# Performance work log

Hardware: AMD Instinct MI355X
Metric: run time of the kernel (lower is better)

Reference implementation:

```python
import jax, jax.numpy as jnp
import numpy as np

EPS = 1e-5
NEG_INF = -9e15  # matches torch's -9000000000000000.0 mask fill


def layer_norm(x, g, b):
    mu = jnp.mean(x, axis=-1, keepdims=True)
    var = jnp.mean((x - mu) ** 2, axis=-1, keepdims=True)
    return (x - mu) / jnp.sqrt(var + EPS) * g + b


def setup_inputs() -> dict:
    key = jax.random.key(0)
    n, C, Cout, K = 8192, 128, 128, 2
    ks = jax.random.split(key, 5)
    x = jax.random.normal(ks[0], (n, C), dtype=jnp.float32)
    adj = jax.random.randint(ks[1], (n, n), 0, 2).astype(jnp.float32)  # 0/1 adjacency
    s = 1.0 / np.sqrt(C)
    # W0[i]: applied as h = x @ W0[i]  (== torch Linear(C,C,bias=False))
    W0 = jax.random.uniform(ks[2], (K, C, C), dtype=jnp.float32, minval=-s, maxval=s)
    W1 = jax.random.uniform(ks[3], (K, C, Cout), dtype=jnp.float32, minval=-s, maxval=s)
    sa = 1.0 / np.sqrt(2 * C)
    a = jax.random.uniform(ks[4], (K, 2 * C), dtype=jnp.float32, minval=-sa, maxval=sa)
    ln1_g = jnp.ones((C,), jnp.float32); ln1_b = jnp.zeros((C,), jnp.float32)
    ln2_g = jnp.ones((C,), jnp.float32); ln2_b = jnp.zeros((C,), jnp.float32)
    return {"x": x, "adj": adj, "W0": W0, "W1": W1, "a": a,
            "ln1_g": ln1_g, "ln1_b": ln1_b, "ln2_g": ln2_g, "ln2_b": ln2_b}


def reference(x, adj, W0, W1, a, ln1_g, ln1_b, ln2_g, ln2_b):
    n, C = x.shape
    K = W0.shape[0]
    Cout = W1.shape[-1]
    # adj + eye (repeated) only feeds `> 0`; equivalent fixed mask:
    mask = (adj > 0) | jnp.eye(n, dtype=bool)
    x_norm = layer_norm(x, ln1_g, ln1_b)
    h_next = jnp.zeros((n, Cout), dtype=x.dtype)
    atten_agg = jnp.zeros((n, n), dtype=x.dtype)
    for i in range(K):
        h = x_norm @ W0[i]                                   # (n, C)
        a_l, a_r = a[i, :C], a[i, C:]
        # h_cross[i,j] = [h[i], h[j]]; linear decomposes exactly:
        e = jax.nn.leaky_relu(h @ a_l[:, None] + (h @ a_r)[None, :])  # (n, n)
        e = jnp.where(mask, e, NEG_INF)
        atten = jax.nn.softmax(e, axis=1)                    # row-stochastic
        attn_h = atten @ h                                   # (n, C)
        attn_h = attn_h + x                                  # residual=True
        attn_h = layer_norm(attn_h, ln2_g, ln2_b)
        h_next = h_next + jax.nn.elu(attn_h @ W1[i]) / K
        atten_agg = atten_agg + atten / K
    return h_next, atten_agg
```

## Files before the change

kernel.cpp:

```cpp
#include <hip/hip_runtime.h>
#include <stdint.h>

#define N 8192
#define C 128

typedef float f32x4 __attribute__((ext_vector_type(4)));
typedef short bf16x8 __attribute__((ext_vector_type(8)));

__device__ __forceinline__ float wred(float v){
#pragma unroll
  for(int o=32;o;o>>=1) v += __shfl_xor(v,o);
  return v;
}
__device__ __forceinline__ unsigned short f2bf(float x){
  union{float f; unsigned u;} c; c.f = x;
  unsigned u = c.u;
  u += 0x7fffu + ((u>>16)&1u);
  return (unsigned short)(u>>16);
}
__device__ __forceinline__ float lrelu(float z){ return z>0.f ? z : 0.01f*z; }

__global__ void k_front(const float* __restrict__ x, const float* __restrict__ g1,
                        const float* __restrict__ b1, const float* __restrict__ W0,
                        const float* __restrict__ a, unsigned short* __restrict__ hB,
                        float* __restrict__ hl, float* __restrict__ hr){
  __shared__ __align__(16) float xn[32*132];
  __shared__ __align__(16) float ws[C*C];
  __shared__ __align__(16) float hs[32*C];
  int t = threadIdx.x, l = t & 63, w = t >> 6;
  int r0 = blockIdx.x*32;
#pragma unroll
  for(int p=0;p<8;p++){
    int row = p*4 + w;
    const float2 xv = *(const float2*)(x + (size_t)(r0+row)*C + l*2);
    float mu = wred(xv.x + xv.y) * (1.f/C);
    float dx = xv.x - mu, dy = xv.y - mu;
    float var = wred(dx*dx + dy*dy) * (1.f/C);
    float rs = rsqrtf(var + 1e-5f);
    const float2 gv = *(const float2*)(g1 + l*2);
    const float2 bv = *(const float2*)(b1 + l*2);
    xn[row*132 + l*2]     = dx*rs*gv.x + bv.x;
    xn[row*132 + l*2 + 1] = dy*rs*gv.y + bv.y;
  }
  int cq = t & 31, rq = t >> 5;
  for(int k=0;k<2;k++){
    __syncthreads();
    const float4* wsrc = (const float4*)(W0 + (size_t)k*C*C);
    float4* wdst = (float4*)ws;
#pragma unroll
    for(int r=0;r<16;r++) wdst[t + r*256] = wsrc[t + r*256];
    __syncthreads();
    float4 acc[4] = {};
    const float4* ws4 = (const float4*)ws;
#pragma unroll 4
    for(int kk=0; kk<C; ++kk){
      float4 wv = ws4[kk*32 + cq];
#pragma unroll
      for(int r=0;r<4;r++){
        float xv = xn[(rq*4+r)*132 + kk];
        acc[r].x += xv*wv.x; acc[r].y += xv*wv.y; acc[r].z += xv*wv.z; acc[r].w += xv*wv.w;
      }
    }
    const float4 al = *(const float4*)(a + k*2*C + cq*4);
    const float4 ar = *(const float4*)(a + k*2*C + C + cq*4);
#pragma unroll
    for(int r=0;r<4;r++){
      float sl = acc[r].x*al.x + acc[r].y*al.y + acc[r].z*al.z + acc[r].w*al.w;
      float sr = acc[r].x*ar.x + acc[r].y*ar.y + acc[r].z*ar.z + acc[r].w*ar.w;
#pragma unroll
      for(int o=16;o;o>>=1){ sl += __shfl_xor(sl,o); sr += __shfl_xor(sr,o); }
      if(cq==0){
        hl[k*N + r0 + rq*4 + r] = sl;
        hr[k*N + r0 + rq*4 + r] = sr;
      }
    }
#pragma unroll
    for(int r=0;r<4;r++) *(float4*)(hs + (rq*4+r)*C + cq*4) = acc[r];
    __syncthreads();
    unsigned short tv[16];
#pragma unroll
    for(int q=0;q<16;q++){
      int f = t*16 + q;
      int cb = f>>9, l2 = (f>>3)&63, tt = f&7;
      tv[q] = f2bf(hs[((l2>>4)*8 + tt)*C + cb*16 + (l2&15)]);
    }
    uint4* dst = (uint4*)(hB + (size_t)(k*256 + blockIdx.x)*4096 + t*16);
    dst[0] = *(uint4*)&tv[0];
    dst[1] = *(uint4*)&tv[8];
  }
}

__global__ void k_denom(const float* __restrict__ adj, const float* __restrict__ hl,
                        const float* __restrict__ hr, float* __restrict__ invd,
                        unsigned char* __restrict__ maskG){
  int t = threadIdx.x, l = t & 63, w = t >> 6;
  int i = blockIdx.x*8 + w;
  float hl0 = hl[i], hl1 = hl[N+i];
  const float4* arow = (const float4*)(adj + (size_t)i*N);
  float s0 = 0.f, s1 = 0.f;
  for(int it=0; it<16; ++it){
    int j0 = it*512 + l*8;
    float4 a0 = arow[j0/4], a1 = arow[j0/4 + 1];
    float4 h00 = *(const float4*)(hr + j0);
    float4 h01 = *(const float4*)(hr + j0 + 4);
    float4 h10 = *(const float4*)(hr + N + j0);
    float4 h11 = *(const float4*)(hr + N + j0 + 4);
    float av[8]  = {a0.x,a0.y,a0.z,a0.w, a1.x,a1.y,a1.z,a1.w};
    float h0v[8] = {h00.x,h00.y,h00.z,h00.w, h01.x,h01.y,h01.z,h01.w};
    float h1v[8] = {h10.x,h10.y,h10.z,h10.w, h11.x,h11.y,h11.z,h11.w};
    unsigned mb = 0;
#pragma unroll
    for(int tt=0; tt<8; ++tt){
      bool m = (av[tt] > 0.f) || (j0+tt == i);
      mb |= ((unsigned)m) << tt;
      float e0 = __expf(lrelu(hl0 + h0v[tt]));
      float e1 = __expf(lrelu(hl1 + h1v[tt]));
      s0 += m ? e0 : 0.f;
      s1 += m ? e1 : 0.f;
    }
    maskG[(size_t)i*1024 + it*64 + l] = (unsigned char)mb;
  }
  s0 = wred(s0); s1 = wred(s1);
  if(l==0){ invd[i] = 1.f/s0; invd[N+i] = 1.f/s1; }
}

__global__ __launch_bounds__(256, 3)
void k_main(const unsigned char* __restrict__ maskG, const float* __restrict__ hl,
            const float* __restrict__ hr, const float* __restrict__ invd,
            const unsigned short* __restrict__ hB,
            float* __restrict__ agg, float* __restrict__ pvp){
  __shared__ __align__(16) uint4 hBs[2][1024];
  __shared__ __align__(16) float hrs[4096];
  int t = threadIdx.x, l = t & 63, w = t >> 6;
  int r0 = blockIdx.x*64, ch = blockIdx.y;
  int g = l >> 4;
  int lr = w*16 + (l & 15);
  int i = r0 + lr;
  {
    int f0 = t*16, k0 = f0 >> 11, j0 = f0 & 2047;
    const float* src = hr + k0*N + ch*2048 + j0;
#pragma unroll
    for(int q=0;q<4;q++) *(float4*)(hrs + f0 + q*4) = *(const float4*)(src + q*4);
  }
  float hl0 = hl[i], hl1 = hl[N+i];
  float id0 = invd[i], id1 = invd[N+i];
  float* grow = agg + (size_t)i*N + ch*2048;
  const unsigned char* mrow = maskG + (size_t)i*1024 + ch*256;
  const uint4* hBu = (const uint4*)hB;
  f32x4 acc[2][8] = {};
  {
    size_t jn = (size_t)(ch*64)*512;
    hBs[0][t]       = hBu[jn + t];
    hBs[0][t + 256] = hBu[jn + t + 256];
    hBs[0][t + 512] = hBu[131072 + jn + t];
    hBs[0][t + 768] = hBu[131072 + jn + t + 256];
  }
  uint4 rB0, rB1, rB2, rB3;
  {
    size_t jn = (size_t)(ch*64 + 1)*512;
    rB0 = hBu[jn + t];           rB1 = hBu[jn + t + 256];
    rB2 = hBu[131072 + jn + t];  rB3 = hBu[131072 + jn + t + 256];
  }
  unsigned mb  = mrow[g];
  unsigned mbn = mrow[4 + g];
  __syncthreads();
  for(int js=0; js<64; ++js){
    int cur = js & 1;
    int jl = js*32 + g*8;
    float4 h00 = *(const float4*)(hrs + jl);
    float4 h01 = *(const float4*)(hrs + jl + 4);
    float4 h10 = *(const float4*)(hrs + 2048 + jl);
    float4 h11 = *(const float4*)(hrs + 2048 + jl + 4);
    float h0v[8] = {h00.x,h00.y,h00.z,h00.w, h01.x,h01.y,h01.z,h01.w};
    float h1v[8] = {h10.x,h10.y,h10.z,h10.w, h11.x,h11.y,h11.z,h11.w};
    float p0[8], p1[8];
#pragma unroll
    for(int tt=0; tt<8; ++tt){
      bool m = (mb >> tt) & 1;
      float e0 = __expf(lrelu(hl0 + h0v[tt]));
      float e1 = __expf(lrelu(hl1 + h1v[tt]));
      p0[tt] = m ? e0 : 0.f;
      p1[tt] = m ? e1 : 0.f;
    }
    float4 g0, g1;
    g0.x = (p0[0]*id0 + p1[0]*id1)*0.5f;
    g0.y = (p0[1]*id0 + p1[1]*id1)*0.5f;
    g0.z = (p0[2]*id0 + p1[2]*id1)*0.5f;
    g0.w = (p0[3]*id0 + p1[3]*id1)*0.5f;
    g1.x = (p0[4]*id0 + p1[4]*id1)*0.5f;
    g1.y = (p0[5]*id0 + p1[5]*id1)*0.5f;
    g1.z = (p0[6]*id0 + p1[6]*id1)*0.5f;
    g1.w = (p0[7]*id0 + p1[7]*id1)*0.5f;
    *(float4*)(grow + jl)     = g0;
    *(float4*)(grow + jl + 4) = g1;
    union { bf16x8 v; unsigned u[4]; } fu0, fu1;
#pragma unroll
    for(int q=0;q<4;q++){
      asm("v_cvt_pk_bf16_f32 %0, %1, %2" : "=v"(fu0.u[q]) : "v"(p0[2*q]), "v"(p0[2*q+1]));
      asm("v_cvt_pk_bf16_f32 %0, %1, %2" : "=v"(fu1.u[q]) : "v"(p1[2*q]), "v"(p1[2*q+1]));
    }
    const unsigned short* bptr = (const unsigned short*)&hBs[cur][0];
#pragma unroll
    for(int cb=0; cb<8; ++cb){
      bf16x8 b0 = *(const bf16x8*)(bptr + (cb*64 + l)*8);
      bf16x8 b1 = *(const bf16x8*)(bptr + 4096 + (cb*64 + l)*8);
      acc[0][cb] = __builtin_amdgcn_mfma_f32_16x16x32_bf16(fu0.v, b0, acc[0][cb], 0, 0, 0);
      acc[1][cb] = __builtin_amdgcn_mfma_f32_16x16x32_bf16(fu1.v, b1, acc[1][cb], 0, 0, 0);
    }
    if(js < 63){
      uint4* dstb = &hBs[cur ^ 1][0];
      dstb[t]       = rB0;
      dstb[t + 256] = rB1;
      dstb[t + 512] = rB2;
      dstb[t + 768] = rB3;
    }
    unsigned mbn2 = 0;
    if(js < 62){
      size_t jn = (size_t)(ch*64 + js + 2)*512;
      rB0 = hBu[jn + t];           rB1 = hBu[jn + t + 256];
      rB2 = hBu[131072 + jn + t];  rB3 = hBu[131072 + jn + t + 256];
      mbn2 = mrow[(js+2)*4 + g];
    }
    mb = mbn; mbn = mbn2;
    __syncthreads();
  }
#pragma unroll
  for(int k=0;k<2;k++)
#pragma unroll
    for(int cb=0;cb<8;cb++)
#pragma unroll
      for(int r=0;r<4;r++){
        int ig = r0 + w*16 + ((l>>4)<<2) + r;
        int c = cb*16 + (l & 15);
        pvp[(size_t)((ch*2 + k)*N + ig)*C + c] = acc[k][cb][r];
      }
}

__global__ void k_reduce_ln(const float* __restrict__ pvp, const float* __restrict__ invd,
                            const float* __restrict__ x, const float* __restrict__ g2,
                            const float* __restrict__ b2, float* __restrict__ tmp){
  int l = threadIdx.x & 63, w = threadIdx.x >> 6;
  int wid = blockIdx.x*4 + w;
  int k = wid >> 13, i = wid & (N-1);
  float s0 = 0.f, s1 = 0.f;
#pragma unroll
  for(int ch=0; ch<4; ++ch){
    const float2 v = *(const float2*)(pvp + (size_t)((ch*2+k)*N + i)*C + l*2);
    s0 += v.x; s1 += v.y;
  }
  float idv = invd[k*N + i];
  const float2 xv = *(const float2*)(x + (size_t)i*C + l*2);
  float a0 = s0*idv + xv.x, a1 = s1*idv + xv.y;
  float mu = wred(a0 + a1) * (1.f/C);
  float d0 = a0 - mu, d1 = a1 - mu;
  float var = wred(d0*d0 + d1*d1) * (1.f/C);
  float rs = rsqrtf(var + 1e-5f);
  const float2 gv = *(const float2*)(g2 + l*2);
  const float2 bv = *(const float2*)(b2 + l*2);
  float2 o; o.x = d0*rs*gv.x + bv.x; o.y = d1*rs*gv.y + bv.y;
  *(float2*)(tmp + (size_t)k*N*C + (size_t)i*C + l*2) = o;
}

__global__ void k_out(const float* __restrict__ tmp, const float* __restrict__ W1,
                      float* __restrict__ out){
  __shared__ __align__(16) float ws[C*C];
  __shared__ __align__(16) float xs[32*132];
  int t = threadIdx.x, r0 = blockIdx.x*32;
  int cq = t & 31, rq = t >> 5;
  float oacc[4][4] = {};
  for(int k=0;k<2;k++){
    __syncthreads();
    const float4* wsrc = (const float4*)(W1 + (size_t)k*C*C);
    float4* wdst = (float4*)ws;
#pragma unroll
    for(int r=0;r<16;r++) wdst[t + r*256] = wsrc[t + r*256];
    const float4* xsrc = (const float4*)(tmp + (size_t)k*N*C + (size_t)r0*C);
#pragma unroll
    for(int r=0;r<4;r++){
      int f = t + r*256;
      int row = f >> 5, c4 = f & 31;
      *(float4*)(xs + row*132 + c4*4) = xsrc[f];
    }
    __syncthreads();
    float4 acc[4] = {};
    const float4* ws4 = (const float4*)ws;
#pragma unroll 4
    for(int kk=0; kk<C; ++kk){
      float4 wv = ws4[kk*32 + cq];
#pragma unroll
      for(int r=0;r<4;r++){
        float xv = xs[(rq*4+r)*132 + kk];
        acc[r].x += xv*wv.x; acc[r].y += xv*wv.y; acc[r].z += xv*wv.z; acc[r].w += xv*wv.w;
      }
    }
#pragma unroll
    for(int r=0;r<4;r++){
      float* ac = (float*)&acc[r];
#pragma unroll
      for(int cc=0;cc<4;cc++){
        float v = ac[cc];
        v = v > 0.f ? v : (__expf(v) - 1.f);
        oacc[r][cc] += 0.5f*v;
      }
    }
  }
#pragma unroll
  for(int r=0;r<4;r++){
    float4 o = make_float4(oacc[r][0], oacc[r][1], oacc[r][2], oacc[r][3]);
    *(float4*)(out + (size_t)(r0+rq*4+r)*C + cq*4) = o;
  }
}

extern "C" void kernel_launch(void* const* d_in, const int* in_sizes, int n_in,
                              void* d_out, int out_size, void* d_ws, size_t ws_size,
                              hipStream_t stream){
  const float* x   = (const float*)d_in[0];
  const float* adj = (const float*)d_in[1];
  const float* W0  = (const float*)d_in[2];
  const float* W1  = (const float*)d_in[3];
  const float* a   = (const float*)d_in[4];
  const float* g1  = (const float*)d_in[5];
  const float* b1  = (const float*)d_in[6];
  const float* g2  = (const float*)d_in[7];
  const float* b2  = (const float*)d_in[8];
  float* out = (float*)d_out;
  float* ws  = (float*)d_ws;

  unsigned short* hB = (unsigned short*)ws;
  float* hl   = ws + 1048576;
  float* hr   = ws + 1064960;
  float* invd = ws + 1081344;
  float* tmp  = ws + 1097728;
  float* pvp  = ws + 3194880;
  unsigned char* maskG = (unsigned char*)(ws + 19972096);
  float* agg  = out + (size_t)N*C;

  k_front    <<<N/32, 256, 0, stream>>>(x, g1, b1, W0, a, hB, hl, hr);
  k_denom    <<<N/8, 512, 0, stream>>>(adj, hl, hr, invd, maskG);
  k_main     <<<dim3(128, 4), 256, 0, stream>>>(maskG, hl, hr, invd, hB, agg, pvp);
  k_reduce_ln<<<(2*N)/4, 256, 0, stream>>>(pvp, invd, x, g2, b2, tmp);
  k_out      <<<N/32, 256, 0, stream>>>(tmp, W1, out);
}
```

Measured before the change: 272.0 us.

## Split k_main column range into eight chunks and lighten the loop barrier

Doubles the column split of the attention-times-h kernel from 4 to 8 chunks, giving 1024 blocks instead of 512 and half the per-block LDS for hr. Occupancy hint rises to 4 blocks per CU. The reduce kernel now sums 8 partials. The loop-end __syncthreads becomes an explicit lgkmcnt wait plus a raw s_barrier, and the last prefetch wraps around instead of being guarded. The cost is twice the partial-output traffic through pvp and one redundant global prefetch at the end of each block.

```diff
diff --git a/kernel.cpp b/kernel.cpp
--- a/kernel.cpp
+++ b/kernel.cpp
@@ -124,53 +124,55 @@
   if(l==0){ invd[i] = 1.f/s0; invd[N+i] = 1.f/s1; }
 }
 
-__global__ __launch_bounds__(256, 3)
+__global__ __launch_bounds__(256, 4)
 void k_main(const unsigned char* __restrict__ maskG, const float* __restrict__ hl,
             const float* __restrict__ hr, const float* __restrict__ invd,
             const unsigned short* __restrict__ hB,
             float* __restrict__ agg, float* __restrict__ pvp){
   __shared__ __align__(16) uint4 hBs[2][1024];
-  __shared__ __align__(16) float hrs[4096];
+  __shared__ __align__(16) float hrs[2048];
   int t = threadIdx.x, l = t & 63, w = t >> 6;
   int r0 = blockIdx.x*64, ch = blockIdx.y;
   int g = l >> 4;
   int lr = w*16 + (l & 15);
   int i = r0 + lr;
   {
-    int f0 = t*16, k0 = f0 >> 11, j0 = f0 & 2047;
-    const float* src = hr + k0*N + ch*2048 + j0;
-#pragma unroll
-    for(int q=0;q<4;q++) *(float4*)(hrs + f0 + q*4) = *(const float4*)(src + q*4);
+    int f0 = t*8, k0 = f0 >> 10, j0 = f0 & 1023;
+    const float* src = hr + k0*N + ch*1024 + j0;
+    *(float4*)(hrs + f0)     = *(const float4*)src;
+    *(float4*)(hrs + f0 + 4) = *(const float4*)(src + 4);
   }
   float hl0 = hl[i], hl1 = hl[N+i];
   float id0 = invd[i], id1 = invd[N+i];
-  float* grow = agg + (size_t)i*N + ch*2048;
-  const unsigned char* mrow = maskG + (size_t)i*1024 + ch*256;
+  float* grow = agg + (size_t)i*N + ch*1024;
+  const unsigned char* mrow = maskG + (size_t)i*1024 + ch*128;
   const uint4* hBu = (const uint4*)hB;
   f32x4 acc[2][8] = {};
-  {
-    size_t jn = (size_t)(ch*64)*512;
-    hBs[0][t]       = hBu[jn + t];
-    hBs[0][t + 256] = hBu[jn + t + 256];
-    hBs[0][t + 512] = hBu[131072 + jn + t];
-    hBs[0][t + 768] = hBu[131072 + jn + t + 256];
-  }
   uint4 rB0, rB1, rB2, rB3;
   {
-    size_t jn = (size_t)(ch*64 + 1)*512;
+    size_t jn = (size_t)(ch*32)*512;
+    rB0 = hBu[jn + t];           rB1 = hBu[jn + t + 256];
+    rB2 = hBu[131072 + jn + t];  rB3 = hBu[131072 + jn + t + 256];
+    hBs[0][t]       = rB0;
+    hBs[0][t + 256] = rB1;
+    hBs[0][t + 512] = rB2;
+    hBs[0][t + 768] = rB3;
+  }
+  {
+    size_t jn = (size_t)(ch*32 + 1)*512;
     rB0 = hBu[jn + t];           rB1 = hBu[jn + t + 256];
     rB2 = hBu[131072 + jn + t];  rB3 = hBu[131072 + jn + t + 256];
   }
   unsigned mb  = mrow[g];
   unsigned mbn = mrow[4 + g];
   __syncthreads();
-  for(int js=0; js<64; ++js){
-    int cur = js & 1;
+  int cur = 0;
+  for(int js=0; js<32; ++js){
     int jl = js*32 + g*8;
     float4 h00 = *(const float4*)(hrs + jl);
     float4 h01 = *(const float4*)(hrs + jl + 4);
-    float4 h10 = *(const float4*)(hrs + 2048 + jl);
-    float4 h11 = *(const float4*)(hrs + 2048 + jl + 4);
+    float4 h10 = *(const float4*)(hrs + 1024 + jl);
+    float4 h11 = *(const float4*)(hrs + 1024 + jl + 4);
     float h0v[8] = {h00.x,h00.y,h00.z,h00.w, h01.x,h01.y,h01.z,h01.w};
     float h1v[8] = {h10.x,h10.y,h10.z,h10.w, h11.x,h11.y,h11.z,h11.w};
     float p0[8], p1[8];
@@ -207,22 +209,27 @@
       acc[0][cb] = __builtin_amdgcn_mfma_f32_16x16x32_bf16(fu0.v, b0, acc[0][cb], 0, 0, 0);
       acc[1][cb] = __builtin_amdgcn_mfma_f32_16x16x32_bf16(fu1.v, b1, acc[1][cb], 0, 0, 0);
     }
-    if(js < 63){
+    if(js < 31){
       uint4* dstb = &hBs[cur ^ 1][0];
       dstb[t]       = rB0;
       dstb[t + 256] = rB1;
       dstb[t + 512] = rB2;
       dstb[t + 768] = rB3;
     }
-    unsigned mbn2 = 0;
-    if(js < 62){
-      size_t jn = (size_t)(ch*64 + js + 2)*512;
+    unsigned mbn2;
+    {
+      int jt = (js + 2) & 31;
+      size_t jn = (size_t)(ch*32 + jt)*512;
       rB0 = hBu[jn + t];           rB1 = hBu[jn + t + 256];
       rB2 = hBu[131072 + jn + t];  rB3 = hBu[131072 + jn + t + 256];
-      mbn2 = mrow[(js+2)*4 + g];
-    }
+      mbn2 = mrow[jt*4 + g];
+    }
+    asm volatile("s_waitcnt lgkmcnt(0)" ::: "memory");
+    __builtin_amdgcn_sched_barrier(0);
+    __builtin_amdgcn_s_barrier();
+    __builtin_amdgcn_sched_barrier(0);
     mb = mbn; mbn = mbn2;
-    __syncthreads();
+    cur ^= 1;
   }
 #pragma unroll
   for(int k=0;k<2;k++)
@@ -244,7 +251,7 @@
   int k = wid >> 13, i = wid & (N-1);
   float s0 = 0.f, s1 = 0.f;
 #pragma unroll
-  for(int ch=0; ch<4; ++ch){
+  for(int ch=0; ch<8; ++ch){
     const float2 v = *(const float2*)(pvp + (size_t)((ch*2+k)*N + i)*C + l*2);
     s0 += v.x; s1 += v.y;
   }
@@ -337,7 +344,7 @@
 
   k_front    <<<N/32, 256, 0, stream>>>(x, g1, b1, W0, a, hB, hl, hr);
   k_denom    <<<N/8, 512, 0, stream>>>(adj, hl, hr, invd, maskG);
-  k_main     <<<dim3(128, 4), 256, 0, stream>>>(maskG, hl, hr, invd, hB, agg, pvp);
+  k_main     <<<dim3(128, 8), 256, 0, stream>>>(maskG, hl, hr, invd, hB, agg, pvp);
   k_reduce_ln<<<(2*N)/4, 256, 0, stream>>>(pvp, invd, x, g2, b2, tmp);
   k_out      <<<N/32, 256, 0, stream>>>(tmp, W1, out);
 }
```

Result: slower. 305.3 us (+12.2%).
